# Performance work log

Hardware: AMD Instinct MI355X
Metric: run time of the kernel (lower is better)

## Reference

```python
import jax, jax.numpy as jnp
import numpy as np

D = 128      # entity_and_theorem_embedding_size
M = 8192     # nodes per tree level
L = 5        # internal (non-leaf) levels
V = 4096     # number of input entities (leaf vocab)
K = 8        # number of binary numerical functions
KL = 4       # number of binary logic functions
G = 4096     # number of ground-truth logic statements


def setup_inputs() -> dict:
    key = jax.random.key(0)
    ks = jax.random.split(key, 16)
    s = 0.05
    return {
        "leaf_ids": jax.random.randint(ks[0], (M,), 0, V, dtype=jnp.int32),
        "left_idx": jax.random.randint(ks[1], (L, M), 0, M, dtype=jnp.int32),
        "right_idx": jax.random.randint(ks[2], (L, M), 0, M, dtype=jnp.int32),
        "nf_fid": jax.random.randint(ks[3], (L, M), 0, K, dtype=jnp.int32),
        "gt_left": jax.random.randint(ks[4], (G,), 0, M, dtype=jnp.int32),
        "gt_right": jax.random.randint(ks[5], (G,), 0, M, dtype=jnp.int32),
        "lf_fid": jax.random.randint(ks[6], (G,), 0, KL, dtype=jnp.int32),
        "emb": jax.random.normal(ks[7], (V, D), jnp.float32),
        "W1": jax.random.normal(ks[8], (K, 2 * D, 4 * D), jnp.float32) * s,
        "b1": jnp.zeros((K, 4 * D), jnp.float32),
        "W2": jax.random.normal(ks[9], (K, 4 * D, 2 * D), jnp.float32) * s,
        "b2": jnp.zeros((K, 2 * D), jnp.float32),
        "W3": jax.random.normal(ks[10], (K, 2 * D, D), jnp.float32) * s,
        "b3": jnp.zeros((K, D), jnp.float32),
        "Wl1": jax.random.normal(ks[11], (KL, 2 * D, 4 * D), jnp.float32) * s,
        "bl1": jnp.zeros((KL, 4 * D), jnp.float32),
        "Wl2": jax.random.normal(ks[12], (KL, 4 * D, D), jnp.float32) * s,
        "bl2": jnp.zeros((KL, D), jnp.float32),
    }


def _select(y, fid):
    # y: [N, K, F], fid: [N] -> [N, F]  (per-node dynamic MLP dispatch)
    return jnp.take_along_axis(y, fid[:, None, None], axis=1)[:, 0, :]


def reference(leaf_ids, left_idx, right_idx, nf_fid, gt_left, gt_right, lf_fid,
              emb, W1, b1, W2, b2, W3, b3, Wl1, bl1, Wl2, bl2):
    # Leaf entities: embedding lookup (input_entity_embedding)
    h0 = emb[leaf_ids]  # [M, D]

    # Internal entity nodes: recursive nf_two2one MLPs, level-synchronous
    def level(h, xs):
        li, ri, fid = xs
        x = jnp.concatenate([h[li], h[ri]], axis=-1)          # [M, 2D] concat of operands
        a1 = jax.nn.relu(jnp.einsum('nd,kdf->nkf', x, W1) + b1)   # [M, K, 4D]
        a2 = jax.nn.relu(jnp.einsum('nkd,kdf->nkf', a1, W2) + b2) # [M, K, 2D]
        a3 = jnp.einsum('nkd,kdf->nkf', a2, W3) + b3              # [M, K, D]
        return _select(a3, fid), None
    hL, _ = jax.lax.scan(level, h0, (left_idx, right_idx, nf_fid))

    # Logic statements: lf_two2one MLP on pairs of entity encodings
    xg = jnp.concatenate([hL[gt_left], hL[gt_right]], axis=-1)    # [G, 2D]
    g1 = jax.nn.relu(jnp.einsum('nd,kdf->nkf', xg, Wl1) + bl1)    # [G, KL, 4D]
    g2 = jnp.einsum('nkd,kdf->nkf', g1, Wl2) + bl2                # [G, KL, D]
    return _select(g2, lf_fid)                                    # [G, D]
```

## Files before the change

kernel.cpp:

```cpp
#include <hip/hip_runtime.h>

constexpr int D  = 128;
constexpr int M  = 8192;
constexpr int L  = 5;
constexpr int K  = 8;
constexpr int KL = 4;
constexpr int G  = 4096;

constexpr int TB   = 64;
constexpr int PADL = M + K * TB;
constexpr int PADG = G + KL * TB;

typedef short bf16x8 __attribute__((ext_vector_type(8)));
typedef float f32x4  __attribute__((ext_vector_type(4)));

__device__ __forceinline__ unsigned short f2bf(float x) {
  union { float f; unsigned int u; } c; c.f = x;
  unsigned int u = c.u + 0x7FFF + ((c.u >> 16) & 1);
  return (unsigned short)(u >> 16);
}
__device__ __forceinline__ float bf2f(unsigned short h) {
  union { unsigned int u; float f; } c; c.u = ((unsigned int)h) << 16;
  return c.f;
}

__device__ __forceinline__ int xcd_swizzle(int b, int n) {
  int q = n >> 3, r = n & 7, xcd = b & 7, off = b >> 3;
  return (xcd < r ? xcd * (q + 1) : r * (q + 1) + (xcd - r) * q) + off;
}

__global__ void leaf_gather_kernel(const int* __restrict__ leaf_ids,
                                   const float* __restrict__ emb,
                                   short* __restrict__ hs) {
  int idx = blockIdx.x * 256 + threadIdx.x;
  int n = idx >> 7, d = idx & 127;
  float w = emb[(size_t)leaf_ids[n] * D + d];
  unsigned short hh = f2bf(w);
  hs[n * 256 + d]       = (short)hh;
  hs[n * 256 + 128 + d] = (short)f2bf(w - bf2f(hh));
}

__global__ void bucket64_kernel(const int* __restrict__ nf_fid,
                                const int* __restrict__ lf_fid,
                                int* __restrict__ orders) {
  int b = blockIdx.x;
  const int* fid; int N, Kf, cap; int* out;
  if (b < L) { fid = nf_fid + b * M; N = M; Kf = K;  cap = PADL; out = orders + b * PADL; }
  else       { fid = lf_fid;         N = G; Kf = KL; cap = PADG; out = orders + L * PADL; }
  __shared__ int cnt[8];
  __shared__ int cur[8];
  int tid = threadIdx.x;
  if (tid < Kf) cnt[tid] = 0;
  __syncthreads();
  for (int i = tid; i < N; i += 256) atomicAdd(&cnt[fid[i]], 1);
  __syncthreads();
  if (tid == 0) {
    int off = 0;
    for (int k = 0; k < Kf; ++k) { cur[k] = off; off += ((cnt[k] + TB - 1) / TB) * TB; }
  }
  __syncthreads();
  for (int i = tid; i < cap; i += 256) out[i] = -1;
  __syncthreads();
  for (int i = tid; i < N; i += 256) {
    int kk = fid[i];
    int pos = atomicAdd(&cur[kk], 1);
    out[pos] = i;
  }
}

__global__ void prep_kernel(const float* __restrict__ W1, const float* __restrict__ W2,
                            const float* __restrict__ W3, const float* __restrict__ Wl1,
                            const float* __restrict__ Wl2,
                            short* __restrict__ B1T, short* __restrict__ B2T,
                            short* __restrict__ B3T, short* __restrict__ BL1T,
                            short* __restrict__ BL2T) {
  int b = blockIdx.x;
  const float* W; short* BT; int KD, F;
  if      (b < 4096) { W = W1;  BT = B1T;  KD = 256; F = 512; }
  else if (b < 6144) { W = W2;  BT = B2T;  KD = 512; F = 256; b -= 4096; }
  else if (b < 7168) { W = W3;  BT = B3T;  KD = 256; F = 128; b -= 6144; }
  else if (b < 9216) { W = Wl1; BT = BL1T; KD = 256; F = 512; b -= 7168; }
  else               { W = Wl2; BT = BL2T; KD = 512; F = 128; b -= 9216; }
  int k = b / F, f = b % F;
  for (int d = threadIdx.x; d < KD; d += 256) {
    float w = W[((size_t)k * KD + d) * F + f];
    unsigned short hi = f2bf(w);
    unsigned short lo = f2bf(w - bf2f(hi));
    BT[((size_t)k * F + f) * (2 * KD) + d]      = (short)hi;
    BT[((size_t)k * F + f) * (2 * KD) + KD + d] = (short)lo;
  }
}

template<int KH, int NN, int EPI, int FUSED, int TROWS>
__global__ __launch_bounds__(256, TROWS == 64 ? 2 : 3) void mfma_gemm(
    const short* __restrict__ A, const short* __restrict__ hsrc,
    const int* __restrict__ gl, const int* __restrict__ gr,
    const short* __restrict__ BT, const float* __restrict__ bias,
    short* __restrict__ Aout, float* __restrict__ outp,
    const int* __restrict__ order, const int* __restrict__ fid) {
  constexpr int BK    = 64;
  constexpr int NCH   = 3 * KH / BK;
  constexpr int LDA   = BK + 8;
  constexpr int RF    = TROWS / 32;
  constexpr int TPR   = 256 / TROWS;
  __shared__ __align__(16) short As[2][TROWS * LDA];
  __shared__ __align__(16) short Bs[2][128 * LDA];
  __shared__ int nodesS[TROWS], liS[TROWS], riS[TROWS];

  const int tid  = threadIdx.x;
  const int bx   = xcd_swizzle(blockIdx.x, gridDim.x);
  const int row0 = bx * TROWS;
  const int ct   = blockIdx.y;

  if (tid < TROWS) {
    int node = order[row0 + tid];
    nodesS[tid] = node;
    if (FUSED) {
      liS[tid] = node >= 0 ? gl[node] : 0;
      riS[tid] = node >= 0 ? gr[node] : 0;
    }
  }
  __syncthreads();
  if (nodesS[0] < 0) return;
  const int kfn = fid[nodesS[0]];
  const short* __restrict__ Bk = BT + (size_t)kfn * NN * (2 * KH);

  const int lane = tid & 63, wave = tid >> 6;
  const int wr = (wave >> 1) * (TROWS / 2);
  const int wc = wave & 1;
  const int l15 = lane & 15, oct = lane >> 4;

  const int ar = tid / TPR;
  const int ag = (tid % TPR) * (BK / TPR);
  const int bn = tid >> 1;
  const int bg = (tid & 1) * 32;

  f32x4 acc[RF][4];
  #pragma unroll
  for (int i = 0; i < RF; ++i)
    #pragma unroll
    for (int j = 0; j < 4; ++j) acc[i][j] = (f32x4)0.f;

  auto loadB_to = [&](int c, int4& r0, int4& r1, int4& r2, int4& r3) {
    int ko = c * BK, seg = ko / KH, wi = ko % KH;
    int pb = (seg == 2) ? KH + wi : wi;
    const int4* p = (const int4*)(Bk + (size_t)(ct * 128 + bn) * (2 * KH) + pb + bg);
    r0 = p[0]; r1 = p[1]; r2 = p[2]; r3 = p[3];
  };
  auto loadA_to = [&](int c, int4& r0, int4& r1) {
    int ko = c * BK, seg = ko / KH, wi = ko % KH;
    int pa = ((seg == 1) ? KH : 0) + wi + ag;
    if (FUSED) {
      int s4 = pa >> 7;
      int node = (s4 & 1) ? riS[ar] : liS[ar];
      if (nodesS[ar] >= 0) {
        const int4* p = (const int4*)(hsrc + (size_t)node * 256 + ((s4 >> 1) << 7) + (pa & 127));
        r0 = p[0];
        if (TPR == 4) r1 = p[1];
      } else {
        r0 = make_int4(0, 0, 0, 0);
        if (TPR == 4) r1 = make_int4(0, 0, 0, 0);
      }
    } else {
      const int4* p = (const int4*)(A + (size_t)(row0 + ar) * (2 * KH) + pa);
      r0 = p[0];
      if (TPR == 4) r1 = p[1];
    }
  };
  auto storeA = [&](int b, const int4& r0, const int4& r1) {
    int4* d4 = (int4*)&As[b][ar * LDA + ag];
    d4[0] = r0;
    if (TPR == 4) d4[1] = r1;
  };
  auto storeB = [&](int b, const int4& r0, const int4& r1, const int4& r2, const int4& r3) {
    int4* db = (int4*)&Bs[b][bn * LDA + bg];
    db[0] = r0; db[1] = r1; db[2] = r2; db[3] = r3;
  };
  auto compute = [&](int b) {
    __builtin_amdgcn_s_setprio(1);
    #pragma unroll
    for (int s = 0; s < 2; ++s) {
      const int ko = s * 32 + oct * 8;
      bf16x8 afr[RF];
      #pragma unroll
      for (int rf = 0; rf < RF; ++rf)
        afr[rf] = *(const bf16x8*)&As[b][(wr + rf * 16 + l15) * LDA + ko];
      #pragma unroll
      for (int cf = 0; cf < 4; ++cf) {
        bf16x8 bb = *(const bf16x8*)&Bs[b][(wc * 64 + cf * 16 + l15) * LDA + ko];
        #pragma unroll
        for (int rf = 0; rf < RF; ++rf)
          acc[rf][cf] = __builtin_amdgcn_mfma_f32_16x16x32_bf16(afr[rf], bb, acc[rf][cf], 0, 0, 0);
      }
    }
    __builtin_amdgcn_s_setprio(0);
  };

  int4 a00, a01, a10, a11;
  int4 b00, b01, b02, b03, b10, b11, b12, b13;
  loadA_to(0, a00, a01); loadB_to(0, b00, b01, b02, b03);
  loadA_to(1, a10, a11); loadB_to(1, b10, b11, b12, b13);
  storeA(0, a00, a01); storeB(0, b00, b01, b02, b03);
  __syncthreads();
  for (int c = 0; c < NCH; c += 2) {
    storeA(1, a10, a11); storeB(1, b10, b11, b12, b13);
    if (c + 2 < NCH) { loadA_to(c + 2, a00, a01); loadB_to(c + 2, b00, b01, b02, b03); }
    compute(0);
    __syncthreads();
    if (c + 2 < NCH) { storeA(0, a00, a01); storeB(0, b00, b01, b02, b03); }
    if (c + 3 < NCH) { loadA_to(c + 3, a10, a11); loadB_to(c + 3, b10, b11, b12, b13); }
    compute(1);
    __syncthreads();
  }

  if (EPI == 0) {
    short* Ls = (short*)&Bs[0][0];
    #pragma unroll
    for (int part = 0; part < 2; ++part) {
      __syncthreads();
      #pragma unroll
      for (int rf = 0; rf < RF; ++rf)
        #pragma unroll
        for (int cf = 0; cf < 4; ++cf) {
          int colL = wc * 64 + cf * 16 + l15;
          float bv = bias[kfn * NN + ct * 128 + colL];
          #pragma unroll
          for (int j = 0; j < 4; ++j) {
            int row = wr + rf * 16 + oct * 4 + j;
            float v = fmaxf(acc[rf][cf][j] + bv, 0.f);
            unsigned short hh = f2bf(v);
            unsigned short val = (part == 0) ? hh : f2bf(v - bf2f(hh));
            Ls[row * 128 + colL] = (short)val;
          }
        }
      __syncthreads();
      constexpr int SPT = TROWS / 2;
      constexpr int TPW = 128 / SPT;
      int row = tid / TPW, sg = (tid % TPW) * SPT;
      const int4* src = (const int4*)&Ls[row * 128 + sg];
      int4* dst = (int4*)&Aout[(size_t)(row0 + row) * (2 * NN) + part * NN + ct * 128 + sg];
      #pragma unroll
      for (int q = 0; q < SPT / 8; ++q) dst[q] = src[q];
    }
  } else if (EPI == 1) {
    float* Lf = (float*)&Bs[0][0];
    #pragma unroll
    for (int h = 0; h < 2; ++h) {
      __syncthreads();
      if (wc == h) {
        #pragma unroll
        for (int rf = 0; rf < RF; ++rf)
          #pragma unroll
          for (int cf = 0; cf < 4; ++cf) {
            int colL = cf * 16 + l15;
            float bv = bias[kfn * 128 + h * 64 + colL];
            #pragma unroll
            for (int j = 0; j < 4; ++j) {
              int row = wr + rf * 16 + oct * 4 + j;
              Lf[row * 64 + colL] = acc[rf][cf][j] + bv;
            }
          }
      }
      __syncthreads();
      constexpr int FPT = TROWS / 4;
      constexpr int TPW = 64 / FPT;
      int row = tid / TPW, off = (tid % TPW) * FPT;
      int node = nodesS[row];
      if (node >= 0) {
        const float4* src = (const float4*)&Lf[row * 64 + off];
        float4* dst = (float4*)&outp[(size_t)node * 128 + h * 64 + off];
        #pragma unroll
        for (int q = 0; q < FPT / 4; ++q) dst[q] = src[q];
      }
    }
  } else {
    short* Ls = (short*)&Bs[0][0];
    #pragma unroll
    for (int rf = 0; rf < RF; ++rf)
      #pragma unroll
      for (int cf = 0; cf < 4; ++cf) {
        int colL = wc * 64 + cf * 16 + l15;
        float bv = bias[kfn * 128 + colL];
        #pragma unroll
        for (int j = 0; j < 4; ++j) {
          int row = wr + rf * 16 + oct * 4 + j;
          float v = acc[rf][cf][j] + bv;
          unsigned short hh = f2bf(v);
          Ls[row * 256 + colL]       = (short)hh;
          Ls[row * 256 + 128 + colL] = (short)f2bf(v - bf2f(hh));
        }
      }
    __syncthreads();
    constexpr int SPT = 256 * TROWS / 256;
    constexpr int TPW = 256 / SPT;
    int row = tid / TPW, sg = (tid % TPW) * SPT;
    int node = nodesS[row];
    if (node >= 0) {
      const int4* src = (const int4*)&Ls[row * 256 + sg];
      int4* dst = (int4*)&Aout[(size_t)node * 256 + sg];
      #pragma unroll
      for (int q = 0; q < SPT / 8; ++q) dst[q] = src[q];
    }
  }
}

extern "C" void kernel_launch(void* const* d_in, const int* in_sizes, int n_in,
                              void* d_out, int out_size, void* d_ws, size_t ws_size,
                              hipStream_t stream) {
  const int*   leaf_ids  = (const int*)d_in[0];
  const int*   left_idx  = (const int*)d_in[1];
  const int*   right_idx = (const int*)d_in[2];
  const int*   nf_fid    = (const int*)d_in[3];
  const int*   gt_left   = (const int*)d_in[4];
  const int*   gt_right  = (const int*)d_in[5];
  const int*   lf_fid    = (const int*)d_in[6];
  const float* emb       = (const float*)d_in[7];
  const float* W1 = (const float*)d_in[8];
  const float* b1 = (const float*)d_in[9];
  const float* W2 = (const float*)d_in[10];
  const float* b2 = (const float*)d_in[11];
  const float* W3 = (const float*)d_in[12];
  const float* b3 = (const float*)d_in[13];
  const float* Wl1 = (const float*)d_in[14];
  const float* bl1 = (const float*)d_in[15];
  const float* Wl2 = (const float*)d_in[16];
  const float* bl2 = (const float*)d_in[17];
  float* out = (float*)d_out;

  const size_t SZ_H    = (size_t)M * 256 * 2;
  const size_t SZ_A1   = (size_t)PADL * 1024 * 2;
  const size_t SZ_A2   = (size_t)PADL * 512 * 2;
  const size_t SZ_B1T  = (size_t)8 * 512 * 512 * 2;
  const size_t SZ_B2T  = (size_t)8 * 256 * 1024 * 2;
  const size_t SZ_B3T  = (size_t)8 * 128 * 512 * 2;
  const size_t SZ_BL1T = (size_t)4 * 512 * 512 * 2;
  const size_t SZ_BL2T = (size_t)4 * 128 * 1024 * 2;

  char* p = (char*)d_ws;
  short* hsA  = (short*)p;  p += SZ_H;
  short* hsB  = (short*)p;  p += SZ_H;
  short* a1s  = (short*)p;  p += SZ_A1;
  short* a2s  = (short*)p;  p += SZ_A2;
  short* B1T  = (short*)p;  p += SZ_B1T;
  short* B2T  = (short*)p;  p += SZ_B2T;
  short* B3T  = (short*)p;  p += SZ_B3T;
  short* BL1T = (short*)p;  p += SZ_BL1T;
  short* BL2T = (short*)p;  p += SZ_BL2T;
  int*   orders = (int*)p;

  leaf_gather_kernel<<<(M * D) / 256, 256, 0, stream>>>(leaf_ids, emb, hsA);
  bucket64_kernel<<<L + 1, 256, 0, stream>>>(nf_fid, lf_fid, orders);
  prep_kernel<<<9728, 256, 0, stream>>>(W1, W2, W3, Wl1, Wl2,
                                        B1T, B2T, B3T, BL1T, BL2T);

  short* hin = hsA;
  short* hout = hsB;
  for (int l = 0; l < L; ++l) {
    const int* ord = orders + l * PADL;
    const int* fidl = nf_fid + l * M;
    mfma_gemm<256, 512, 0, 1, 64><<<dim3(PADL / 64, 4), 256, 0, stream>>>(
        nullptr, hin, left_idx + l * M, right_idx + l * M,
        B1T, b1, a1s, nullptr, ord, fidl);
    mfma_gemm<512, 256, 0, 0, 64><<<dim3(PADL / 64, 2), 256, 0, stream>>>(
        a1s, nullptr, nullptr, nullptr,
        B2T, b2, a2s, nullptr, ord, fidl);
    mfma_gemm<256, 128, 2, 0, 32><<<dim3(PADL / 32, 1), 256, 0, stream>>>(
        a2s, nullptr, nullptr, nullptr,
        B3T, b3, hout, nullptr, ord, fidl);
    short* t = hin; hin = hout; hout = t;
  }
  const int* ordG = orders + L * PADL;
  mfma_gemm<256, 512, 0, 1, 64><<<dim3(PADG / 64, 4), 256, 0, stream>>>(
      nullptr, hin, gt_left, gt_right,
      BL1T, bl1, a1s, nullptr, ordG, lf_fid);
  mfma_gemm<512, 128, 1, 0, 32><<<dim3(PADG / 32, 1), 256, 0, stream>>>(
      a1s, nullptr, nullptr, nullptr,
      BL2T, bl2, nullptr, out, ordG, lf_fid);
}
```

Before: 462.3 us.

## Deepen GEMM register prefetch to three stages with a single LDS barrier per chunk

Restructures the main K-loop of the MFMA GEMM so each chunk's global loads are issued three chunks ahead into a 3-slot register ring. Each iteration stores the next chunk to shared memory, launches a new load and computes, then crosses one barrier written as inline asm that waits only on lgkmcnt instead of a full __syncthreads. The loop is fully unrolled. Launch bounds are unified to a minimum of 2 waves per EU, which gives the 32-row variant more registers for the extra prefetch slots but may lower its occupancy. The goal is to hide global-memory latency behind more in-flight loads, at the cost of register pressure and possible spills.

```diff
diff --git a/kernel.cpp b/kernel.cpp
--- a/kernel.cpp
+++ b/kernel.cpp
@@ -92,7 +92,7 @@
 }
 
 template<int KH, int NN, int EPI, int FUSED, int TROWS>
-__global__ __launch_bounds__(256, TROWS == 64 ? 2 : 3) void mfma_gemm(
+__global__ __launch_bounds__(256, 2) void mfma_gemm(
     const short* __restrict__ A, const short* __restrict__ hsrc,
     const int* __restrict__ gl, const int* __restrict__ gr,
     const short* __restrict__ BT, const float* __restrict__ bias,
@@ -141,40 +141,43 @@
     #pragma unroll
     for (int j = 0; j < 4; ++j) acc[i][j] = (f32x4)0.f;
 
-  auto loadB_to = [&](int c, int4& r0, int4& r1, int4& r2, int4& r3) {
-    int ko = c * BK, seg = ko / KH, wi = ko % KH;
-    int pb = (seg == 2) ? KH + wi : wi;
-    const int4* p = (const int4*)(Bk + (size_t)(ct * 128 + bn) * (2 * KH) + pb + bg);
-    r0 = p[0]; r1 = p[1]; r2 = p[2]; r3 = p[3];
+  int4 sa[3][2];
+  int4 sb[3][4];
+
+  auto loadC = [&](int s, int c) {
+    {
+      int ko = c * BK, seg = ko / KH, wi = ko % KH;
+      int pb = (seg == 2) ? KH + wi : wi;
+      const int4* p = (const int4*)(Bk + (size_t)(ct * 128 + bn) * (2 * KH) + pb + bg);
+      sb[s][0] = p[0]; sb[s][1] = p[1]; sb[s][2] = p[2]; sb[s][3] = p[3];
+    }
+    {
+      int ko = c * BK, seg = ko / KH, wi = ko % KH;
+      int pa = ((seg == 1) ? KH : 0) + wi + ag;
+      if (FUSED) {
+        int s4 = pa >> 7;
+        int node = (s4 & 1) ? riS[ar] : liS[ar];
+        if (nodesS[ar] >= 0) {
+          const int4* p = (const int4*)(hsrc + (size_t)node * 256 + ((s4 >> 1) << 7) + (pa & 127));
+          sa[s][0] = p[0];
+          if (TPR == 4) sa[s][1] = p[1];
+        } else {
+          sa[s][0] = make_int4(0, 0, 0, 0);
+          if (TPR == 4) sa[s][1] = make_int4(0, 0, 0, 0);
+        }
+      } else {
+        const int4* p = (const int4*)(A + (size_t)(row0 + ar) * (2 * KH) + pa);
+        sa[s][0] = p[0];
+        if (TPR == 4) sa[s][1] = p[1];
+      }
+    }
   };
-  auto loadA_to = [&](int c, int4& r0, int4& r1) {
-    int ko = c * BK, seg = ko / KH, wi = ko % KH;
-    int pa = ((seg == 1) ? KH : 0) + wi + ag;
-    if (FUSED) {
-      int s4 = pa >> 7;
-      int node = (s4 & 1) ? riS[ar] : liS[ar];
-      if (nodesS[ar] >= 0) {
-        const int4* p = (const int4*)(hsrc + (size_t)node * 256 + ((s4 >> 1) << 7) + (pa & 127));
-        r0 = p[0];
-        if (TPR == 4) r1 = p[1];
-      } else {
-        r0 = make_int4(0, 0, 0, 0);
-        if (TPR == 4) r1 = make_int4(0, 0, 0, 0);
-      }
-    } else {
-      const int4* p = (const int4*)(A + (size_t)(row0 + ar) * (2 * KH) + pa);
-      r0 = p[0];
-      if (TPR == 4) r1 = p[1];
-    }
-  };
-  auto storeA = [&](int b, const int4& r0, const int4& r1) {
+  auto storeC = [&](int s, int b) {
     int4* d4 = (int4*)&As[b][ar * LDA + ag];
-    d4[0] = r0;
-    if (TPR == 4) d4[1] = r1;
-  };
-  auto storeB = [&](int b, const int4& r0, const int4& r1, const int4& r2, const int4& r3) {
+    d4[0] = sa[s][0];
+    if (TPR == 4) d4[1] = sa[s][1];
     int4* db = (int4*)&Bs[b][bn * LDA + bg];
-    db[0] = r0; db[1] = r1; db[2] = r2; db[3] = r3;
+    db[0] = sb[s][0]; db[1] = sb[s][1]; db[2] = sb[s][2]; db[3] = sb[s][3];
   };
   auto compute = [&](int b) {
     __builtin_amdgcn_s_setprio(1);
@@ -195,22 +198,21 @@
     }
     __builtin_amdgcn_s_setprio(0);
   };
-
-  int4 a00, a01, a10, a11;
-  int4 b00, b01, b02, b03, b10, b11, b12, b13;
-  loadA_to(0, a00, a01); loadB_to(0, b00, b01, b02, b03);
-  loadA_to(1, a10, a11); loadB_to(1, b10, b11, b12, b13);
-  storeA(0, a00, a01); storeB(0, b00, b01, b02, b03);
-  __syncthreads();
-  for (int c = 0; c < NCH; c += 2) {
-    storeA(1, a10, a11); storeB(1, b10, b11, b12, b13);
-    if (c + 2 < NCH) { loadA_to(c + 2, a00, a01); loadB_to(c + 2, b00, b01, b02, b03); }
-    compute(0);
-    __syncthreads();
-    if (c + 2 < NCH) { storeA(0, a00, a01); storeB(0, b00, b01, b02, b03); }
-    if (c + 3 < NCH) { loadA_to(c + 3, a10, a11); loadB_to(c + 3, b10, b11, b12, b13); }
-    compute(1);
-    __syncthreads();
+  auto lds_barrier = [&]() {
+    asm volatile("s_waitcnt lgkmcnt(0)\n\ts_barrier" ::: "memory");
+  };
+
+  loadC(0, 0); loadC(1, 1); loadC(2, 2);
+  storeC(0, 0);
+  loadC(0, 3);
+  lds_barrier();
+
+  #pragma unroll
+  for (int c = 0; c < NCH; ++c) {
+    if (c + 1 < NCH) storeC((c + 1) % 3, (c + 1) & 1);
+    if (c + 4 < NCH) loadC((c + 1) % 3, c + 4);
+    compute(c & 1);
+    lds_barrier();
   }
 
   if (EPI == 0) {
@@ -291,7 +293,7 @@
         }
       }
     __syncthreads();
-    constexpr int SPT = 256 * TROWS / 256;
+    constexpr int SPT = TROWS;
     constexpr int TPW = 256 / SPT;
     int row = tid / TPW, sg = (tid % TPW) * SPT;
     int node = nodesS[row];
```

Measured after the change: 1.015 ms. 119% more time.
